# Kernel optimization log

Measured on AMD Instinct MI355X. Metric: run time of the kernel, lower is better.

The kernel has to match this reference:

```python
import jax, jax.numpy as jnp
import numpy as np

T_DIFF = 1000.0
LN_EPS = 1e-5


def _lin(x, w, b):
    return jnp.matmul(x, w.T) + b


def _ln(x, g, b):
    m = jnp.mean(x, axis=-1, keepdims=True)
    v = jnp.mean((x - m) ** 2, axis=-1, keepdims=True)
    return (x - m) / jnp.sqrt(v + LN_EPS) * g + b


def _pos_lin(x, w, b):
    return jnp.matmul(x, jax.nn.softplus(w).T) + b


def _gamma(t, g_l1_w, g_l1_b, g_l2_w, g_l2_b, g_l3_w, g_l3_b, gamma_0, gamma_1):
    def gtilde(u):
        l1 = _pos_lin(u, g_l1_w, g_l1_b)
        return l1 + _pos_lin(jax.nn.sigmoid(_pos_lin(l1, g_l2_w, g_l2_b)), g_l3_w, g_l3_b)
    g0, g1, gt = gtilde(jnp.zeros_like(t)), gtilde(jnp.ones_like(t)), gtilde(t)
    return gamma_0 + (gamma_1 - gamma_0) * (gt - g0) / (g1 - g0)


def _pair_dist(a):
    # safe pairwise euclidean distances, (B,N,N,1)
    diff = a[:, :, None, :] - a[:, None, :, :]
    d2 = jnp.sum(diff * diff, axis=-1, keepdims=True)
    return diff, jnp.sqrt(jnp.maximum(d2, 1e-12)), d2


def _egc_layer(x, h, x0, p):
    _, d0, _ = _pair_dist(x0)                      # original distances
    diff, dist, d2 = _pair_dist(x)                 # current distances (pre-LN x)
    h = _ln(h, p['lnh_g'], p['lnh_b'])
    x = _ln(x, p['lnx_g'], p['lnx_b'])
    B, N, F = h.shape
    h_i = jnp.broadcast_to(h[:, :, None, :], (B, N, N, F))
    h_j = jnp.broadcast_to(h[:, None, :, :], (B, N, N, F))
    einp = jnp.concatenate([h_i, h_j, d2, d0], axis=-1)  # (B,N,N,2F+2)
    m = jax.nn.silu(_lin(einp, p['edg1_w'], p['edg1_b']))
    m = jax.nn.silu(_lin(m, p['edg2_w'], p['edg2_b']))
    e = jax.nn.sigmoid(_lin(m, p['edgi_w'], p['edgi_b']))
    e = e * (1.0 - jnp.eye(N, dtype=e.dtype)[None, :, :, None])
    m_agg = jnp.sum(e * m, axis=2)                 # sum over j -> (B,N,F)
    hn = jax.nn.silu(_lin(jnp.concatenate([h, m_agg], axis=-1), p['node1_w'], p['node1_b']))
    hn = h + _lin(hn, p['node2_w'], p['node2_b'])
    cw = jax.nn.silu(_lin(einp, p['cor1_w'], p['cor1_b']))
    cw = jax.nn.silu(_lin(cw, p['cor2_w'], p['cor2_b']))
    cw = _lin(cw, p['cor3_w'], p['cor3_b'])        # (B,N,N,1)
    x_next = x + jnp.sum(cw * (diff / (dist + 1.0)), axis=2)
    return x_next, hn


def setup_inputs() -> dict:
    key = jax.random.key(0)
    ks = iter(jax.random.split(key, 64))
    B, N, H, L = 8, 192, 32, 4
    d = {}
    d['xyz_atom_species'] = jax.random.normal(next(ks), (B, N, 4), jnp.float32)
    d['pdf'] = jax.random.normal(next(ks), (B, 3000), jnp.float32)
    d['t'] = jax.random.uniform(next(ks), (B,), jnp.float32) * T_DIFF

    def w(k, shape):
        fan_in = shape[-1]
        return jax.random.normal(k, shape, jnp.float32) / np.sqrt(fan_in)

    d['emb_in_w'] = w(next(ks), (H, 12)); d['emb_in_b'] = jnp.zeros((H,), jnp.float32)
    d['emb_out_w'] = w(next(ks), (1, H)); d['emb_out_b'] = jnp.zeros((1,), jnp.float32)
    d['x_out_w'] = w(next(ks), (3, 3)); d['x_out_b'] = jnp.zeros((3,), jnp.float32)
    d['pdf_w'] = w(next(ks), (10, 3000)); d['pdf_b'] = jnp.zeros((10,), jnp.float32)
    d['g_l1_w'] = w(next(ks), (1, 1)); d['g_l1_b'] = jnp.zeros((1,), jnp.float32)
    d['g_l2_w'] = w(next(ks), (1024, 1)); d['g_l2_b'] = jnp.zeros((1024,), jnp.float32)
    d['g_l3_w'] = w(next(ks), (1, 1024)); d['g_l3_b'] = jnp.zeros((1,), jnp.float32)
    d['gamma_0'] = jnp.array([-5.0], jnp.float32)
    d['gamma_1'] = jnp.array([10.0], jnp.float32)
    d['lnh_g'] = jnp.ones((L, H), jnp.float32); d['lnh_b'] = jnp.zeros((L, H), jnp.float32)
    d['lnx_g'] = jnp.ones((L, 3), jnp.float32); d['lnx_b'] = jnp.zeros((L, 3), jnp.float32)
    d['edg1_w'] = w(next(ks), (L, H, 2 * H + 2)); d['edg1_b'] = jnp.zeros((L, H), jnp.float32)
    d['edg2_w'] = w(next(ks), (L, H, H)); d['edg2_b'] = jnp.zeros((L, H), jnp.float32)
    d['edgi_w'] = w(next(ks), (L, 1, H)); d['edgi_b'] = jnp.zeros((L, 1), jnp.float32)
    d['node1_w'] = w(next(ks), (L, H, 2 * H)); d['node1_b'] = jnp.zeros((L, H), jnp.float32)
    d['node2_w'] = w(next(ks), (L, H, H)); d['node2_b'] = jnp.zeros((L, H), jnp.float32)
    d['cor1_w'] = w(next(ks), (L, H, 2 * H + 2)); d['cor1_b'] = jnp.zeros((L, H), jnp.float32)
    d['cor2_w'] = w(next(ks), (L, H, H)); d['cor2_b'] = jnp.zeros((L, H), jnp.float32)
    d['cor3_w'] = w(next(ks), (L, 1, H)); d['cor3_b'] = jnp.zeros((L, 1), jnp.float32)
    return d


def reference(xyz_atom_species, pdf, t, emb_in_w, emb_in_b, emb_out_w, emb_out_b,
              x_out_w, x_out_b, pdf_w, pdf_b, g_l1_w, g_l1_b, g_l2_w, g_l2_b,
              g_l3_w, g_l3_b, gamma_0, gamma_1, lnh_g, lnh_b, lnx_g, lnx_b,
              edg1_w, edg1_b, edg2_w, edg2_b, edgi_w, edgi_b, node1_w, node1_b,
              node2_w, node2_b, cor1_w, cor1_b, cor2_w, cor2_b, cor3_w, cor3_b):
    B, N, _ = xyz_atom_species.shape
    h = xyz_atom_species[:, :, 3:4]                # (B,N,1)
    x = xyz_atom_species[:, :, :3]
    x0 = x
    tn = (t / T_DIFF)[:, None]                     # (B,1)
    t_emb = _gamma(tn, g_l1_w, g_l1_b, g_l2_w, g_l2_b, g_l3_w, g_l3_b, gamma_0, gamma_1)
    pdf_emb = _lin(pdf, pdf_w, pdf_b)              # (B,10)
    h = jnp.concatenate([
        h,
        jnp.broadcast_to(t_emb[:, None, :], (B, N, 1)),
        jnp.broadcast_to(pdf_emb[:, None, :], (B, N, 10)),
    ], axis=-1)
    h = _lin(h, emb_in_w, emb_in_b)                # (B,N,32)
    for l in range(4):
        p = dict(lnh_g=lnh_g[l], lnh_b=lnh_b[l], lnx_g=lnx_g[l], lnx_b=lnx_b[l],
                 edg1_w=edg1_w[l], edg1_b=edg1_b[l], edg2_w=edg2_w[l], edg2_b=edg2_b[l],
                 edgi_w=edgi_w[l], edgi_b=edgi_b[l], node1_w=node1_w[l], node1_b=node1_b[l],
                 node2_w=node2_w[l], node2_b=node2_b[l], cor1_w=cor1_w[l], cor1_b=cor1_b[l],
                 cor2_w=cor2_w[l], cor2_b=cor2_b[l], cor3_w=cor3_w[l], cor3_b=cor3_b[l])
        x, h = _egc_layer(x, h, x0, p)
    h = _lin(h, emb_out_w, emb_out_b)
    x = _lin(x, x_out_w, x_out_b) - x0
    return jnp.concatenate([x, h], axis=-1)        # (B,N,4)
```

## Files before the change

kernel.cpp:

```cpp
#include <hip/hip_runtime.h>
#include <hip/hip_bf16.h>
#include <math.h>

#define BATCH 8
#define NATOMS 192
#define HF 32

using short8 = __attribute__((ext_vector_type(8))) short;
using f32x4  = __attribute__((ext_vector_type(4))) float;

__device__ __forceinline__ float fast_rcp(float x){ return __builtin_amdgcn_rcpf(x); }
__device__ __forceinline__ float sigmoid_f(float x){ return fast_rcp(1.0f+__expf(-x)); }
__device__ __forceinline__ float silu_f(float x){ return x*fast_rcp(1.0f+__expf(-x)); }
__device__ __forceinline__ float softplus_f(float x){ return fmaxf(x,0.0f)+log1pf(expf(-fabsf(x))); }
__device__ __forceinline__ unsigned short f2bf(float x){
  __hip_bfloat16 h = __float2bfloat16(x);
  return __builtin_bit_cast(unsigned short, h);
}

__device__ __forceinline__ float wave_sum(float v){
  v += __shfl_xor(v, 1);
  v += __shfl_xor(v, 2);
  v += __shfl_xor(v, 4);
  v += __shfl_xor(v, 8);
  v += __shfl_xor(v, 16);
  v += __shfl_xor(v, 32);
  return v;
}

__global__ __launch_bounds__(256) void k_prelude(
    const float* __restrict__ pdf, const float* __restrict__ t,
    const float* __restrict__ pdf_w, const float* __restrict__ pdf_b,
    const float* __restrict__ g1w, const float* __restrict__ g1b,
    const float* __restrict__ g2w, const float* __restrict__ g2b,
    const float* __restrict__ g3w, const float* __restrict__ g3b,
    const float* __restrict__ gamma0, const float* __restrict__ gamma1,
    float* __restrict__ temb, float* __restrict__ pdfe)
{
  __shared__ float lds[4];
  const int bx = blockIdx.x, tid = threadIdx.x;
  const int wv = tid >> 6, ln = tid & 63;

  if (bx < 80){
    const int b = bx / 10, o = bx % 10;
    const float* pb = pdf + b*3000;
    const float* wb = pdf_w + o*3000;
    float p = 0.f;
    for (int k = tid; k < 3000; k += 256) p = fmaf(pb[k], wb[k], p);
    p = wave_sum(p);
    if (ln == 0) lds[wv] = p;
    __syncthreads();
    if (tid == 0) pdfe[b*10 + o] = lds[0] + lds[1] + lds[2] + lds[3] + pdf_b[o];
    return;
  }
  const int b = bx - 80;
  const float w1 = softplus_f(g1w[0]);
  const float b1 = g1b[0];
  const float tn = t[b] * (1.0f/1000.0f);
  const float l1_0 = b1;
  const float l1_1 = w1 + b1;
  const float l1_t = fmaf(w1, tn, b1);
  float a0 = 0.f, a1 = 0.f, at = 0.f;
  for (int k = tid; k < 1024; k += 256){
    float w2 = softplus_f(g2w[k]);
    float bb = g2b[k];
    float w3 = softplus_f(g3w[k]);
    a0 += sigmoid_f(fmaf(w2, l1_0, bb)) * w3;
    a1 += sigmoid_f(fmaf(w2, l1_1, bb)) * w3;
    at += sigmoid_f(fmaf(w2, l1_t, bb)) * w3;
  }
  float sums[3]; float vals[3] = {a0, a1, at};
  for (int r = 0; r < 3; ++r){
    float v = wave_sum(vals[r]);
    __syncthreads();
    if (ln == 0) lds[wv] = v;
    __syncthreads();
    sums[r] = lds[0] + lds[1] + lds[2] + lds[3];
  }
  if (tid == 0){
    const float b3 = g3b[0];
    const float g0 = l1_0 + sums[0] + b3;
    const float g1v = l1_1 + sums[1] + b3;
    const float gt = l1_t + sums[2] + b3;
    temb[b] = gamma0[0] + (gamma1[0] - gamma0[0]) * (gt - g0) / (g1v - g0);
  }
}

__global__ __launch_bounds__(256) void k_embed(
    const float* __restrict__ xyz, const float* __restrict__ temb,
    const float* __restrict__ pdfe, const float* __restrict__ wi,
    const float* __restrict__ bi, float* __restrict__ h, float* __restrict__ x)
{
  int g = blockIdx.x * 256 + threadIdx.x;
  if (g >= BATCH*NATOMS*HF) return;
  int f = g & 31;
  int node = g >> 5;
  int b = node / NATOMS;
  float sp = xyz[node*4 + 3];
  const float* w = wi + f*12;
  float a = bi[f];
  a = fmaf(sp, w[0], a);
  a = fmaf(temb[b], w[1], a);
  const float* pe = pdfe + b*10;
#pragma unroll
  for (int p = 0; p < 10; ++p) a = fmaf(pe[p], w[2+p], a);
  h[node*32 + f] = a;
  if (f < 3) x[node*3 + f] = xyz[node*4 + f];
}

__global__ __launch_bounds__(256) void k_wprep(
    const float* __restrict__ e2w, const float* __restrict__ c2w,
    unsigned short* __restrict__ e2wb, unsigned short* __restrict__ c2wb)
{
  int g = blockIdx.x*256 + threadIdx.x;
  if (g < 4096){
    e2wb[g] = f2bf(e2w[g]);
    c2wb[g] = f2bf(c2w[g]);
  }
}

__global__ __launch_bounds__(256) void k_node(
    const float* __restrict__ hraw,
    const float* __restrict__ lnhg, const float* __restrict__ lnhb,
    const float* __restrict__ e1w, const float* __restrict__ e1b,
    const float* __restrict__ c1w, const float* __restrict__ c1b,
    float* __restrict__ hln, float* __restrict__ ue, float* __restrict__ uc,
    float* __restrict__ vep, float* __restrict__ vcp)
{
  int g = blockIdx.x * 256 + threadIdx.x;
  if (g >= BATCH*NATOMS*32) return;
  const int f = g & 31, node = g >> 5;
  const float* row = hraw + node*32;
  float hl[32];
  float m = 0.f;
#pragma unroll
  for (int k = 0; k < 32; ++k){ hl[k] = row[k]; m += hl[k]; }
  m *= (1.0f/32.0f);
  float v = 0.f;
#pragma unroll
  for (int k = 0; k < 32; ++k){ float d = hl[k]-m; v = fmaf(d, d, v); }
  float r = rsqrtf(v*(1.0f/32.0f) + 1e-5f);
#pragma unroll
  for (int k = 0; k < 32; ++k) hl[k] = fmaf((hl[k]-m)*r, lnhg[k], lnhb[k]);
  hln[node*32 + f] = hl[f];

  const float* we = e1w + f*66;
  float sv = e1b[f], su = 0.f;
#pragma unroll
  for (int k = 0; k < 32; ++k){ sv = fmaf(hl[k], we[k], sv); su = fmaf(hl[k], we[32+k], su); }
  vep[node*32 + f] = sv;
  ue [node*32 + f] = su;

  const float* wc = c1w + f*66;
  float cv = c1b[f], cu = 0.f;
#pragma unroll
  for (int k = 0; k < 32; ++k){ cv = fmaf(hl[k], wc[k], cv); cu = fmaf(hl[k], wc[32+k], cu); }
  vcp[node*32 + f] = cv;
  uc [node*32 + f] = cu;
}

__global__ __launch_bounds__(128, 3) void k_pair(
    const float* __restrict__ xin, const float* __restrict__ xyz,
    const float* __restrict__ ue, const float* __restrict__ uc,
    const float* __restrict__ vep, const float* __restrict__ vcp,
    const float* __restrict__ e1w, const float* __restrict__ c1w,
    const unsigned short* __restrict__ e2wb, const unsigned short* __restrict__ c2wb,
    const float* __restrict__ e2b, const float* __restrict__ eiw,
    const float* __restrict__ eib,
    const float* __restrict__ c2b, const float* __restrict__ c3w,
    const float* __restrict__ c3b,
    float* __restrict__ pm, float* __restrict__ pxc)
{
  __shared__ float s_geo[64][6];
  __shared__ unsigned short s_m1[64][40];
  __shared__ unsigned short s_c1[64][40];
  __shared__ unsigned short s_we[32][40];
  __shared__ unsigned short s_wc[32][40];

  const int i = blockIdx.x, b = blockIdx.y, chunk = blockIdx.z;
  const int tid = threadIdx.x;
  const int base = b * NATOMS;

  if (tid < 64){
    const int jj = tid;
    const int j = chunk*64 + jj;
    const float* xi_p = xin + (base + i)*3;
    const float* xj_p = xin + (base + j)*3;
    const float dfx = xi_p[0] - xj_p[0], dfy = xi_p[1] - xj_p[1], dfz = xi_p[2] - xj_p[2];
    const float d2 = dfx*dfx + dfy*dfy + dfz*dfz;
    const float dist = sqrtf(fmaxf(d2, 1e-12f));
    const float* x0i = xyz + (base + i)*4;
    const float* x0j = xyz + (base + j)*4;
    const float q0 = x0i[0]-x0j[0], q1 = x0i[1]-x0j[1], q2 = x0i[2]-x0j[2];
    const float d0 = sqrtf(fmaxf(q0*q0 + q1*q1 + q2*q2, 1e-12f));
    s_geo[jj][0] = dfx; s_geo[jj][1] = dfy; s_geo[jj][2] = dfz;
    s_geo[jj][3] = d2;  s_geo[jj][4] = d0;  s_geo[jj][5] = dist;
  } else {
    const int u = tid - 64;
    const short8* es = (const short8*)e2wb;
    const short8* cs = (const short8*)c2wb;
#pragma unroll
    for (int h = 0; h < 2; ++h){
      const int c = u + h*64;
      const int f = c >> 2, kq = c & 3;
      *(short8*)&s_we[f][kq*8] = es[c];
      *(short8*)&s_wc[f][kq*8] = cs[c];
    }
  }
  __syncthreads();

  {
    const int k = tid & 31, jg = tid >> 5;
    const float vpe = vep[(base + i)*32 + k];
    const float vpc = vcp[(base + i)*32 + k];
    const float we64 = e1w[k*66 + 64], we65 = e1w[k*66 + 65];
    const float wc64 = c1w[k*66 + 64], wc65 = c1w[k*66 + 65];
#pragma unroll
    for (int jj = jg; jj < 64; jj += 4){
      const float d2 = s_geo[jj][3], d0 = s_geo[jj][4];
      const int j = chunk*64 + jj;
      const float uev = ue[(size_t)(base + j)*32 + k];
      const float m1 = silu_f(fmaf(d2, we64, fmaf(d0, we65, vpe + uev)));
      s_m1[jj][k] = f2bf(m1);
      const float ucv = uc[(size_t)(base + j)*32 + k];
      const float c1 = silu_f(fmaf(d2, wc64, fmaf(d0, wc65, vpc + ucv)));
      s_c1[jj][k] = f2bf(c1);
    }
  }
  __syncthreads();

  const int lane = tid & 63;
  const int n = lane & 15, quad = lane >> 4;

  if (tid < 64){
    short8 b0 = *(const short8*)&s_we[n][quad*8];
    short8 b1 = *(const short8*)&s_we[16 + n][quad*8];
    f32x4 acc0[4], acc1[4];
#pragma unroll
    for (int jt = 0; jt < 4; ++jt){
      short8 a = *(const short8*)&s_m1[jt*16 + n][quad*8];
      f32x4 z = {0.f, 0.f, 0.f, 0.f};
      acc0[jt] = __builtin_amdgcn_mfma_f32_16x16x32_bf16(a, b0, z, 0, 0, 0);
      acc1[jt] = __builtin_amdgcn_mfma_f32_16x16x32_bf16(a, b1, z, 0, 0, 0);
    }
    const float eb0 = e2b[n], eb1 = e2b[16 + n];
    const float ew0 = eiw[n], ew1 = eiw[16 + n];
    const float ebias = eib[0];
    float ma0 = 0.f, ma1 = 0.f;
#pragma unroll
    for (int jt = 0; jt < 4; ++jt){
      float m20[4], m21[4], g[4];
#pragma unroll
      for (int r = 0; r < 4; ++r){
        m20[r] = silu_f(acc0[jt][r] + eb0);
        m21[r] = silu_f(acc1[jt][r] + eb1);
        g[r] = m20[r]*ew0 + m21[r]*ew1;
      }
#pragma unroll
      for (int r = 0; r < 4; ++r){
        g[r] += __shfl_xor(g[r], 1);
        g[r] += __shfl_xor(g[r], 2);
        g[r] += __shfl_xor(g[r], 4);
        g[r] += __shfl_xor(g[r], 8);
      }
#pragma unroll
      for (int r = 0; r < 4; ++r){
        const int jglob = chunk*64 + jt*16 + quad*4 + r;
        const float e = (jglob == i) ? 0.0f : sigmoid_f(g[r] + ebias);
        ma0 = fmaf(e, m20[r], ma0);
        ma1 = fmaf(e, m21[r], ma1);
      }
    }
    ma0 += __shfl_xor(ma0, 16); ma0 += __shfl_xor(ma0, 32);
    ma1 += __shfl_xor(ma1, 16); ma1 += __shfl_xor(ma1, 32);
    if (lane < 16){
      float* o = pm + ((size_t)(base + i)*3 + chunk)*32;
      o[lane] = ma0;
      o[16 + lane] = ma1;
    }
  } else {
    short8 b0 = *(const short8*)&s_wc[n][quad*8];
    short8 b1 = *(const short8*)&s_wc[16 + n][quad*8];
    f32x4 acc0[4], acc1[4];
#pragma unroll
    for (int jt = 0; jt < 4; ++jt){
      short8 a = *(const short8*)&s_c1[jt*16 + n][quad*8];
      f32x4 z = {0.f, 0.f, 0.f, 0.f};
      acc0[jt] = __builtin_amdgcn_mfma_f32_16x16x32_bf16(a, b0, z, 0, 0, 0);
      acc1[jt] = __builtin_amdgcn_mfma_f32_16x16x32_bf16(a, b1, z, 0, 0, 0);
    }
    const float cb0 = c2b[n], cb1 = c2b[16 + n];
    const float cw0 = c3w[n], cw1 = c3w[16 + n];
    const float cbias = c3b[0];
    float px = 0.f, py = 0.f, pz = 0.f;
#pragma unroll
    for (int jt = 0; jt < 4; ++jt){
      float g[4];
#pragma unroll
      for (int r = 0; r < 4; ++r){
        g[r] = silu_f(acc0[jt][r] + cb0)*cw0 + silu_f(acc1[jt][r] + cb1)*cw1;
      }
#pragma unroll
      for (int r = 0; r < 4; ++r){
        g[r] += __shfl_xor(g[r], 1);
        g[r] += __shfl_xor(g[r], 2);
        g[r] += __shfl_xor(g[r], 4);
        g[r] += __shfl_xor(g[r], 8);
      }
#pragma unroll
      for (int r = 0; r < 4; ++r){
        const int jj = jt*16 + quad*4 + r;
        const float s = (g[r] + cbias) * fast_rcp(s_geo[jj][5] + 1.0f);
        px = fmaf(s, s_geo[jj][0], px);
        py = fmaf(s, s_geo[jj][1], py);
        pz = fmaf(s, s_geo[jj][2], pz);
      }
    }
    px += __shfl_xor(px, 16); px += __shfl_xor(px, 32);
    py += __shfl_xor(py, 16); py += __shfl_xor(py, 32);
    pz += __shfl_xor(pz, 16); pz += __shfl_xor(pz, 32);
    if (lane == 0){
      float* o = pxc + ((size_t)(base + i)*3 + chunk)*3;
      o[0] = px; o[1] = py; o[2] = pz;
    }
  }
}

__global__ __launch_bounds__(256) void k_post(
    float* hln, const float* __restrict__ xin,
    const float* __restrict__ pm, const float* __restrict__ pxc,
    float* __restrict__ hout, float* __restrict__ xout,
    const float* __restrict__ n1w, const float* __restrict__ n1b,
    const float* __restrict__ n2w, const float* __restrict__ n2b,
    const float* __restrict__ lnxg, const float* __restrict__ lnxb,
    const float* __restrict__ lnhg_n, const float* __restrict__ lnhb_n,
    const float* __restrict__ e1w_n, const float* __restrict__ e1b_n,
    const float* __restrict__ c1w_n, const float* __restrict__ c1b_n,
    float* __restrict__ ue, float* __restrict__ uc,
    float* __restrict__ vep, float* __restrict__ vcp)
{
  __shared__ float s_hl[8][33];
  __shared__ float s_mg[8][33];
  __shared__ float s_n1[8][33];
  __shared__ float s_ho[8][33];

  const int tid = threadIdx.x;
  const int il = tid >> 5, f = tid & 31;
  const int node = blockIdx.x*8 + il;

  const float hlf = hln[node*32 + f];
  s_hl[il][f] = hlf;
  const float* pmn = pm + (size_t)node*96;
  s_mg[il][f] = pmn[f] + pmn[32 + f] + pmn[64 + f];
  __syncthreads();

  float a = n1b[f];
  const float* w1 = n1w + f*64;
#pragma unroll
  for (int k = 0; k < 32; ++k) a = fmaf(s_hl[il][k], w1[k], a);
#pragma unroll
  for (int k = 0; k < 32; ++k) a = fmaf(s_mg[il][k], w1[32+k], a);
  s_n1[il][f] = silu_f(a);

  if (f < 3){
    const float* xr = xin + node*3;
    const float x0 = xr[0], x1 = xr[1], x2 = xr[2];
    const float mx = (x0 + x1 + x2) * (1.0f/3.0f);
    const float v0 = x0-mx, v1 = x1-mx, v2 = x2-mx;
    const float r = rsqrtf((v0*v0 + v1*v1 + v2*v2)*(1.0f/3.0f) + 1e-5f);
    const float xv = (f == 0) ? x0 : ((f == 1) ? x1 : x2);
    const float xl = fmaf((xv - mx)*r, lnxg[f], lnxb[f]);
    const float* pc = pxc + (size_t)node*9;
    xout[node*3 + f] = xl + pc[f] + pc[3 + f] + pc[6 + f];
  }
  __syncthreads();

  float o = n2b[f];
  const float* w2 = n2w + f*32;
#pragma unroll
  for (int k = 0; k < 32; ++k) o = fmaf(s_n1[il][k], w2[k], o);
  const float ho = hlf + o;
  hout[node*32 + f] = ho;
  s_ho[il][f] = ho;
  __syncthreads();

  float m = 0.f;
#pragma unroll
  for (int k = 0; k < 32; ++k) m += s_ho[il][k];
  m *= (1.0f/32.0f);
  float v = 0.f;
#pragma unroll
  for (int k = 0; k < 32; ++k){ float d = s_ho[il][k]-m; v = fmaf(d, d, v); }
  const float r = rsqrtf(v*(1.0f/32.0f) + 1e-5f);
  float hl[32];
#pragma unroll
  for (int k = 0; k < 32; ++k) hl[k] = fmaf((s_ho[il][k]-m)*r, lnhg_n[k], lnhb_n[k]);
  hln[node*32 + f] = hl[f];

  const float* we = e1w_n + f*66;
  float sv = e1b_n[f], su = 0.f;
#pragma unroll
  for (int k = 0; k < 32; ++k){ sv = fmaf(hl[k], we[k], sv); su = fmaf(hl[k], we[32+k], su); }
  vep[node*32 + f] = sv;
  ue [node*32 + f] = su;

  const float* wc = c1w_n + f*66;
  float cv = c1b_n[f], cu = 0.f;
#pragma unroll
  for (int k = 0; k < 32; ++k){ cv = fmaf(hl[k], wc[k], cv); cu = fmaf(hl[k], wc[32+k], cu); }
  vcp[node*32 + f] = cv;
  uc [node*32 + f] = cu;
}

__global__ __launch_bounds__(256) void k_final(
    const float* __restrict__ hin, const float* __restrict__ xin,
    const float* __restrict__ xyz,
    const float* __restrict__ how, const float* __restrict__ hob,
    const float* __restrict__ xow, const float* __restrict__ xob,
    float* __restrict__ out)
{
  int g = blockIdx.x * 256 + threadIdx.x;
  if (g >= BATCH*NATOMS) return;
  const float* h = hin + g*32;
  float a = hob[0];
#pragma unroll
  for (int k = 0; k < 32; ++k) a = fmaf(h[k], how[k], a);
  const float* x = xin + g*3;
#pragma unroll
  for (int c = 0; c < 3; ++c){
    float o = xob[c];
    o = fmaf(x[0], xow[c*3+0], o);
    o = fmaf(x[1], xow[c*3+1], o);
    o = fmaf(x[2], xow[c*3+2], o);
    out[g*4 + c] = o - xyz[g*4 + c];
  }
  out[g*4 + 3] = a;
}

extern "C" void kernel_launch(void* const* d_in, const int* in_sizes, int n_in,
                              void* d_out, int out_size, void* d_ws, size_t ws_size,
                              hipStream_t stream)
{
  const float* xyz      = (const float*)d_in[0];
  const float* pdf      = (const float*)d_in[1];
  const float* t        = (const float*)d_in[2];
  const float* emb_in_w = (const float*)d_in[3];
  const float* emb_in_b = (const float*)d_in[4];
  const float* emb_out_w= (const float*)d_in[5];
  const float* emb_out_b= (const float*)d_in[6];
  const float* x_out_w  = (const float*)d_in[7];
  const float* x_out_b  = (const float*)d_in[8];
  const float* pdf_w    = (const float*)d_in[9];
  const float* pdf_b    = (const float*)d_in[10];
  const float* g1w      = (const float*)d_in[11];
  const float* g1b      = (const float*)d_in[12];
  const float* g2w      = (const float*)d_in[13];
  const float* g2b      = (const float*)d_in[14];
  const float* g3w      = (const float*)d_in[15];
  const float* g3b      = (const float*)d_in[16];
  const float* gamma0   = (const float*)d_in[17];
  const float* gamma1   = (const float*)d_in[18];
  const float* lnhg     = (const float*)d_in[19];
  const float* lnhb     = (const float*)d_in[20];
  const float* lnxg     = (const float*)d_in[21];
  const float* lnxb     = (const float*)d_in[22];
  const float* e1w      = (const float*)d_in[23];
  const float* e1b      = (const float*)d_in[24];
  const float* e2w      = (const float*)d_in[25];
  const float* e2b      = (const float*)d_in[26];
  const float* eiw      = (const float*)d_in[27];
  const float* eib      = (const float*)d_in[28];
  const float* n1w      = (const float*)d_in[29];
  const float* n1b      = (const float*)d_in[30];
  const float* n2w      = (const float*)d_in[31];
  const float* n2b      = (const float*)d_in[32];
  const float* c1w      = (const float*)d_in[33];
  const float* c1b      = (const float*)d_in[34];
  const float* c2w      = (const float*)d_in[35];
  const float* c2b      = (const float*)d_in[36];
  const float* c3w      = (const float*)d_in[37];
  const float* c3b      = (const float*)d_in[38];

  const int NTOT = BATCH*NATOMS;
  float* ws   = (float*)d_ws;
  float* temb = ws;
  float* pdfe = ws + 8;
  unsigned short* e2wb = (unsigned short*)(ws + 96);
  unsigned short* c2wb = e2wb + 4096;
  float* h0   = ws + 96 + 4096;
  float* hout = h0   + NTOT*32;
  float* xb0  = hout + NTOT*32;
  float* xb1  = xb0  + NTOT*3;
  float* hln  = xb1  + NTOT*3;
  float* ue   = hln  + NTOT*32;
  float* uc   = ue   + NTOT*32;
  float* vep  = uc   + NTOT*32;
  float* vcp  = vep  + NTOT*32;
  float* pm   = vcp  + NTOT*32;
  float* pxc  = pm   + NTOT*96;

  k_prelude<<<88, 256, 0, stream>>>(pdf, t, pdf_w, pdf_b,
      g1w, g1b, g2w, g2b, g3w, g3b, gamma0, gamma1, temb, pdfe);
  k_embed<<<(NTOT*HF + 255)/256, 256, 0, stream>>>(
      xyz, temb, pdfe, emb_in_w, emb_in_b, h0, xb0);
  k_wprep<<<16, 256, 0, stream>>>(e2w, c2w, e2wb, c2wb);
  k_node<<<(NTOT*32 + 255)/256, 256, 0, stream>>>(
      h0, lnhg, lnhb, e1w, e1b, c1w, c1b, hln, ue, uc, vep, vcp);

  const float* xcur = xb0; float* xnext = xb1;
  for (int l = 0; l < 4; ++l){
    const int n = (l < 3) ? (l + 1) : 3;
    k_pair<<<dim3(NATOMS, BATCH, 3), 128, 0, stream>>>(
        xcur, xyz, ue, uc, vep, vcp,
        e1w + l*2112, c1w + l*2112,
        e2wb + l*1024, c2wb + l*1024,
        e2b + l*32, eiw + l*32, eib + l,
        c2b + l*32, c3w + l*32, c3b + l,
        pm, pxc);
    k_post<<<NTOT/8, 256, 0, stream>>>(
        hln, xcur, pm, pxc, hout, xnext,
        n1w + l*2048, n1b + l*32, n2w + l*1024, n2b + l*32,
        lnxg + l*3, lnxb + l*3,
        lnhg + n*32, lnhb + n*32, e1w + n*2112, e1b + n*32,
        c1w + n*2112, c1b + n*32,
        ue, uc, vep, vcp);
    const float* tx = xcur; xcur = xnext; xnext = (float*)tx;
  }

  k_final<<<(NTOT + 255)/256, 256, 0, stream>>>(
      hout, xcur, xyz, emb_out_w, emb_out_b, x_out_w, x_out_b, (float*)d_out);
}
```

Before: 274.9 us.

## Fuse node update into pair kernel via last-block atomic counter, merge prelude kernels

After: 926.0 us. 237% more time.

```diff
diff --git a/kernel.cpp b/kernel.cpp
--- a/kernel.cpp
+++ b/kernel.cpp
@@ -35,12 +35,20 @@
     const float* __restrict__ g2w, const float* __restrict__ g2b,
     const float* __restrict__ g3w, const float* __restrict__ g3b,
     const float* __restrict__ gamma0, const float* __restrict__ gamma1,
+    const float* __restrict__ e2w, const float* __restrict__ c2w,
+    unsigned short* __restrict__ e2wb, unsigned short* __restrict__ c2wb,
     float* __restrict__ temb, float* __restrict__ pdfe)
 {
   __shared__ float lds[4];
   const int bx = blockIdx.x, tid = threadIdx.x;
   const int wv = tid >> 6, ln = tid & 63;
 
+  if (bx >= 88){
+    const int g = (bx - 88)*256 + tid;
+    e2wb[g] = f2bf(e2w[g]);
+    c2wb[g] = f2bf(c2w[g]);
+    return;
+  }
   if (bx < 80){
     const int b = bx / 10, o = bx % 10;
     const float* pb = pdf + b*3000;
@@ -86,55 +94,43 @@
   }
 }
 
-__global__ __launch_bounds__(256) void k_embed(
+__global__ __launch_bounds__(256) void k_embed_node(
     const float* __restrict__ xyz, const float* __restrict__ temb,
     const float* __restrict__ pdfe, const float* __restrict__ wi,
-    const float* __restrict__ bi, float* __restrict__ h, float* __restrict__ x)
-{
-  int g = blockIdx.x * 256 + threadIdx.x;
-  if (g >= BATCH*NATOMS*HF) return;
-  int f = g & 31;
-  int node = g >> 5;
-  int b = node / NATOMS;
-  float sp = xyz[node*4 + 3];
-  const float* w = wi + f*12;
-  float a = bi[f];
-  a = fmaf(sp, w[0], a);
-  a = fmaf(temb[b], w[1], a);
-  const float* pe = pdfe + b*10;
-#pragma unroll
-  for (int p = 0; p < 10; ++p) a = fmaf(pe[p], w[2+p], a);
-  h[node*32 + f] = a;
-  if (f < 3) x[node*3 + f] = xyz[node*4 + f];
-}
-
-__global__ __launch_bounds__(256) void k_wprep(
-    const float* __restrict__ e2w, const float* __restrict__ c2w,
-    unsigned short* __restrict__ e2wb, unsigned short* __restrict__ c2wb)
-{
-  int g = blockIdx.x*256 + threadIdx.x;
-  if (g < 4096){
-    e2wb[g] = f2bf(e2w[g]);
-    c2wb[g] = f2bf(c2w[g]);
-  }
-}
-
-__global__ __launch_bounds__(256) void k_node(
-    const float* __restrict__ hraw,
+    const float* __restrict__ bi,
     const float* __restrict__ lnhg, const float* __restrict__ lnhb,
     const float* __restrict__ e1w, const float* __restrict__ e1b,
     const float* __restrict__ c1w, const float* __restrict__ c1b,
-    float* __restrict__ hln, float* __restrict__ ue, float* __restrict__ uc,
-    float* __restrict__ vep, float* __restrict__ vcp)
+    float* __restrict__ x, float* __restrict__ hln,
+    float* __restrict__ ue, float* __restrict__ uc,
+    float* __restrict__ vep, float* __restrict__ vcp,
+    int* __restrict__ cnt)
 {
-  int g = blockIdx.x * 256 + threadIdx.x;
-  if (g >= BATCH*NATOMS*32) return;
-  const int f = g & 31, node = g >> 5;
-  const float* row = hraw + node*32;
+  __shared__ float s_h[8][33];
+  const int tid = threadIdx.x;
+  const int il = tid >> 5, f = tid & 31;
+  const int node = blockIdx.x*8 + il;
+  const int b = node / NATOMS;
+
+  {
+    const float sp = xyz[node*4 + 3];
+    const float* w = wi + f*12;
+    float a = bi[f];
+    a = fmaf(sp, w[0], a);
+    a = fmaf(temb[b], w[1], a);
+    const float* pe = pdfe + b*10;
+#pragma unroll
+    for (int p = 0; p < 10; ++p) a = fmaf(pe[p], w[2+p], a);
+    s_h[il][f] = a;
+  }
+  if (f < 3) x[node*3 + f] = xyz[node*4 + f];
+  if (f == 0) cnt[node] = 0;
+  __syncthreads();
+
   float hl[32];
   float m = 0.f;
 #pragma unroll
-  for (int k = 0; k < 32; ++k){ hl[k] = row[k]; m += hl[k]; }
+  for (int k = 0; k < 32; ++k){ hl[k] = s_h[il][k]; m += hl[k]; }
   m *= (1.0f/32.0f);
   float v = 0.f;
 #pragma unroll
@@ -161,21 +157,35 @@
 
 __global__ __launch_bounds__(128, 3) void k_pair(
     const float* __restrict__ xin, const float* __restrict__ xyz,
-    const float* __restrict__ ue, const float* __restrict__ uc,
-    const float* __restrict__ vep, const float* __restrict__ vcp,
+    const float* __restrict__ hln, const float* __restrict__ ue,
+    const float* __restrict__ uc, const float* __restrict__ vep,
+    const float* __restrict__ vcp,
     const float* __restrict__ e1w, const float* __restrict__ c1w,
     const unsigned short* __restrict__ e2wb, const unsigned short* __restrict__ c2wb,
     const float* __restrict__ e2b, const float* __restrict__ eiw,
     const float* __restrict__ eib,
     const float* __restrict__ c2b, const float* __restrict__ c3w,
     const float* __restrict__ c3b,
-    float* __restrict__ pm, float* __restrict__ pxc)
+    const float* __restrict__ n1w, const float* __restrict__ n1b,
+    const float* __restrict__ n2w, const float* __restrict__ n2b,
+    const float* __restrict__ lnxg, const float* __restrict__ lnxb,
+    const float* __restrict__ lnhg_n, const float* __restrict__ lnhb_n,
+    const float* __restrict__ e1w_n, const float* __restrict__ e1b_n,
+    const float* __restrict__ c1w_n, const float* __restrict__ c1b_n,
+    float* __restrict__ hln_n, float* __restrict__ ue_n,
+    float* __restrict__ uc_n, float* __restrict__ vep_n,
+    float* __restrict__ vcp_n, float* __restrict__ xout,
+    const float* __restrict__ how, const float* __restrict__ hob,
+    const float* __restrict__ xow, const float* __restrict__ xob,
+    float* __restrict__ dout, const int lastl,
+    float* __restrict__ pm, float* __restrict__ pxc, int* __restrict__ cnt)
 {
   __shared__ float s_geo[64][6];
   __shared__ unsigned short s_m1[64][40];
   __shared__ unsigned short s_c1[64][40];
   __shared__ unsigned short s_we[32][40];
   __shared__ unsigned short s_wc[32][40];
+  __shared__ int s_last;
 
   const int i = blockIdx.x, b = blockIdx.y, chunk = blockIdx.z;
   const int tid = threadIdx.x;
@@ -324,117 +334,99 @@
       o[0] = px; o[1] = py; o[2] = pz;
     }
   }
-}
-
-__global__ __launch_bounds__(256) void k_post(
-    float* hln, const float* __restrict__ xin,
-    const float* __restrict__ pm, const float* __restrict__ pxc,
-    float* __restrict__ hout, float* __restrict__ xout,
-    const float* __restrict__ n1w, const float* __restrict__ n1b,
-    const float* __restrict__ n2w, const float* __restrict__ n2b,
-    const float* __restrict__ lnxg, const float* __restrict__ lnxb,
-    const float* __restrict__ lnhg_n, const float* __restrict__ lnhb_n,
-    const float* __restrict__ e1w_n, const float* __restrict__ e1b_n,
-    const float* __restrict__ c1w_n, const float* __restrict__ c1b_n,
-    float* __restrict__ ue, float* __restrict__ uc,
-    float* __restrict__ vep, float* __restrict__ vcp)
-{
-  __shared__ float s_hl[8][33];
-  __shared__ float s_mg[8][33];
-  __shared__ float s_n1[8][33];
-  __shared__ float s_ho[8][33];
-
-  const int tid = threadIdx.x;
-  const int il = tid >> 5, f = tid & 31;
-  const int node = blockIdx.x*8 + il;
-
+
+  __threadfence();
+  if (tid == 0){
+    const int old = atomicAdd(&cnt[base + i], 1);
+    s_last = (old == 2) ? 1 : 0;
+  }
+  __syncthreads();
+  if (!s_last) return;
+  if (tid >= 64) return;
+  __threadfence();
+
+  const int f = tid & 31;
+  const int node = base + i;
+
+  const float* pmn = pm + (size_t)node*96;
+  const float mgf = pmn[f] + pmn[32 + f] + pmn[64 + f];
   const float hlf = hln[node*32 + f];
-  s_hl[il][f] = hlf;
-  const float* pmn = pm + (size_t)node*96;
-  s_mg[il][f] = pmn[f] + pmn[32 + f] + pmn[64 + f];
-  __syncthreads();
 
   float a = n1b[f];
   const float* w1 = n1w + f*64;
 #pragma unroll
-  for (int k = 0; k < 32; ++k) a = fmaf(s_hl[il][k], w1[k], a);
-#pragma unroll
-  for (int k = 0; k < 32; ++k) a = fmaf(s_mg[il][k], w1[32+k], a);
-  s_n1[il][f] = silu_f(a);
-
-  if (f < 3){
+  for (int k = 0; k < 32; ++k) a = fmaf(__shfl(hlf, k, 64), w1[k], a);
+#pragma unroll
+  for (int k = 0; k < 32; ++k) a = fmaf(__shfl(mgf, k, 64), w1[32 + k], a);
+  const float n1v = silu_f(a);
+  float o = n2b[f];
+  const float* w2 = n2w + f*32;
+#pragma unroll
+  for (int k = 0; k < 32; ++k) o = fmaf(__shfl(n1v, k, 64), w2[k], o);
+  const float ho = hlf + o;
+
+  float xn0, xn1, xn2;
+  {
     const float* xr = xin + node*3;
     const float x0 = xr[0], x1 = xr[1], x2 = xr[2];
     const float mx = (x0 + x1 + x2) * (1.0f/3.0f);
     const float v0 = x0-mx, v1 = x1-mx, v2 = x2-mx;
     const float r = rsqrtf((v0*v0 + v1*v1 + v2*v2)*(1.0f/3.0f) + 1e-5f);
-    const float xv = (f == 0) ? x0 : ((f == 1) ? x1 : x2);
-    const float xl = fmaf((xv - mx)*r, lnxg[f], lnxb[f]);
     const float* pc = pxc + (size_t)node*9;
-    xout[node*3 + f] = xl + pc[f] + pc[3 + f] + pc[6 + f];
-  }
-  __syncthreads();
-
-  float o = n2b[f];
-  const float* w2 = n2w + f*32;
-#pragma unroll
-  for (int k = 0; k < 32; ++k) o = fmaf(s_n1[il][k], w2[k], o);
-  const float ho = hlf + o;
-  hout[node*32 + f] = ho;
-  s_ho[il][f] = ho;
-  __syncthreads();
-
-  float m = 0.f;
-#pragma unroll
-  for (int k = 0; k < 32; ++k) m += s_ho[il][k];
-  m *= (1.0f/32.0f);
-  float v = 0.f;
-#pragma unroll
-  for (int k = 0; k < 32; ++k){ float d = s_ho[il][k]-m; v = fmaf(d, d, v); }
-  const float r = rsqrtf(v*(1.0f/32.0f) + 1e-5f);
-  float hl[32];
-#pragma unroll
-  for (int k = 0; k < 32; ++k) hl[k] = fmaf((s_ho[il][k]-m)*r, lnhg_n[k], lnhb_n[k]);
-  hln[node*32 + f] = hl[f];
-
-  const float* we = e1w_n + f*66;
-  float sv = e1b_n[f], su = 0.f;
-#pragma unroll
-  for (int k = 0; k < 32; ++k){ sv = fmaf(hl[k], we[k], sv); su = fmaf(hl[k], we[32+k], su); }
-  vep[node*32 + f] = sv;
-  ue [node*32 + f] = su;
-
-  const float* wc = c1w_n + f*66;
-  float cv = c1b_n[f], cu = 0.f;
-#pragma unroll
-  for (int k = 0; k < 32; ++k){ cv = fmaf(hl[k], wc[k], cv); cu = fmaf(hl[k], wc[32+k], cu); }
-  vcp[node*32 + f] = cv;
-  uc [node*32 + f] = cu;
-}
-
-__global__ __launch_bounds__(256) void k_final(
-    const float* __restrict__ hin, const float* __restrict__ xin,
-    const float* __restrict__ xyz,
-    const float* __restrict__ how, const float* __restrict__ hob,
-    const float* __restrict__ xow, const float* __restrict__ xob,
-    float* __restrict__ out)
-{
-  int g = blockIdx.x * 256 + threadIdx.x;
-  if (g >= BATCH*NATOMS) return;
-  const float* h = hin + g*32;
-  float a = hob[0];
-#pragma unroll
-  for (int k = 0; k < 32; ++k) a = fmaf(h[k], how[k], a);
-  const float* x = xin + g*3;
-#pragma unroll
-  for (int c = 0; c < 3; ++c){
-    float o = xob[c];
-    o = fmaf(x[0], xow[c*3+0], o);
-    o = fmaf(x[1], xow[c*3+1], o);
-    o = fmaf(x[2], xow[c*3+2], o);
-    out[g*4 + c] = o - xyz[g*4 + c];
-  }
-  out[g*4 + 3] = a;
+    xn0 = fmaf(v0*r, lnxg[0], lnxb[0]) + pc[0] + pc[3] + pc[6];
+    xn1 = fmaf(v1*r, lnxg[1], lnxb[1]) + pc[1] + pc[4] + pc[7];
+    xn2 = fmaf(v2*r, lnxg[2], lnxb[2]) + pc[2] + pc[5] + pc[8];
+  }
+
+  if (!lastl){
+    if (tid == 0){
+      float* xo = xout + node*3;
+      xo[0] = xn0; xo[1] = xn1; xo[2] = xn2;
+    }
+    float s = ho;
+    s += __shfl_xor(s, 1); s += __shfl_xor(s, 2); s += __shfl_xor(s, 4);
+    s += __shfl_xor(s, 8); s += __shfl_xor(s, 16);
+    const float m = s * (1.0f/32.0f);
+    const float d = ho - m;
+    float vv = d*d;
+    vv += __shfl_xor(vv, 1); vv += __shfl_xor(vv, 2); vv += __shfl_xor(vv, 4);
+    vv += __shfl_xor(vv, 8); vv += __shfl_xor(vv, 16);
+    const float r = rsqrtf(vv*(1.0f/32.0f) + 1e-5f);
+    const float hl = fmaf(d*r, lnhg_n[f], lnhb_n[f]);
+    if (tid < 32) hln_n[node*32 + f] = hl;
+
+    const float* we = e1w_n + f*66;
+    const float* wc = c1w_n + f*66;
+    float sv = e1b_n[f], su = 0.f, cv = c1b_n[f], cu = 0.f;
+#pragma unroll
+    for (int k = 0; k < 32; ++k){
+      const float tkk = __shfl(hl, k, 64);
+      sv = fmaf(tkk, we[k], sv);
+      su = fmaf(tkk, we[32 + k], su);
+      cv = fmaf(tkk, wc[k], cv);
+      cu = fmaf(tkk, wc[32 + k], cu);
+    }
+    if (tid < 32){
+      vep_n[node*32 + f] = sv;
+      ue_n [node*32 + f] = su;
+      vcp_n[node*32 + f] = cv;
+      uc_n [node*32 + f] = cu;
+    }
+  } else {
+    float hh = how[f] * ho;
+    hh += __shfl_xor(hh, 1); hh += __shfl_xor(hh, 2); hh += __shfl_xor(hh, 4);
+    hh += __shfl_xor(hh, 8); hh += __shfl_xor(hh, 16);
+    if (tid == 0) dout[node*4 + 3] = hh + hob[0];
+    if (tid < 3){
+      const int c = tid;
+      float oo = xob[c];
+      oo = fmaf(xn0, xow[c*3 + 0], oo);
+      oo = fmaf(xn1, xow[c*3 + 1], oo);
+      oo = fmaf(xn2, xow[c*3 + 2], oo);
+      dout[node*4 + c] = oo - xyz[node*4 + c];
+    }
+  }
+  if (tid == 0) cnt[node] = 0;
 }
 
 extern "C" void kernel_launch(void* const* d_in, const int* in_sizes, int n_in,
@@ -487,46 +479,48 @@
   float* pdfe = ws + 8;
   unsigned short* e2wb = (unsigned short*)(ws + 96);
   unsigned short* c2wb = e2wb + 4096;
-  float* h0   = ws + 96 + 4096;
-  float* hout = h0   + NTOT*32;
-  float* xb0  = hout + NTOT*32;
-  float* xb1  = xb0  + NTOT*3;
-  float* hln  = xb1  + NTOT*3;
-  float* ue   = hln  + NTOT*32;
-  float* uc   = ue   + NTOT*32;
-  float* vep  = uc   + NTOT*32;
-  float* vcp  = vep  + NTOT*32;
-  float* pm   = vcp  + NTOT*32;
+  float* p0   = ws + 96 + 4096;
+  float* xbA  = p0;                float* xbB  = xbA + NTOT*3;
+  float* hlnA = xbB  + NTOT*3;     float* hlnB = hlnA + NTOT*32;
+  float* ueA  = hlnB + NTOT*32;    float* ueB  = ueA  + NTOT*32;
+  float* ucA  = ueB  + NTOT*32;    float* ucB  = ucA  + NTOT*32;
+  float* vepA = ucB  + NTOT*32;    float* vepB = vepA + NTOT*32;
+  float* vcpA = vepB + NTOT*32;    float* vcpB = vcpA + NTOT*32;
+  float* pm   = vcpB + NTOT*32;
   float* pxc  = pm   + NTOT*96;
-
-  k_prelude<<<88, 256, 0, stream>>>(pdf, t, pdf_w, pdf_b,
-      g1w, g1b, g2w, g2b, g3w, g3b, gamma0, gamma1, temb, pdfe);
-  k_embed<<<(NTOT*HF + 255)/256, 256, 0, stream>>>(
-      xyz, temb, pdfe, emb_in_w, emb_in_b, h0, xb0);
-  k_wprep<<<16, 256, 0, stream>>>(e2w, c2w, e2wb, c2wb);
-  k_node<<<(NTOT*32 + 255)/256, 256, 0, stream>>>(
-      h0, lnhg, lnhb, e1w, e1b, c1w, c1b, hln, ue, uc, vep, vcp);
-
-  const float* xcur = xb0; float* xnext = xb1;
+  int*   cnt  = (int*)(pxc + NTOT*9);
+
+  float* xb[2]  = {xbA,  xbB};
+  float* hlnP[2]= {hlnA, hlnB};
+  float* ueP[2] = {ueA,  ueB};
+  float* ucP[2] = {ucA,  ucB};
+  float* vepP[2]= {vepA, vepB};
+  float* vcpP[2]= {vcpA, vcpB};
+
+  k_prelude<<<104, 256, 0, stream>>>(pdf, t, pdf_w, pdf_b,
+      g1w, g1b, g2w, g2b, g3w, g3b, gamma0, gamma1,
+      e2w, c2w, e2wb, c2wb, temb, pdfe);
+  k_embed_node<<<NTOT/8, 256, 0, stream>>>(
+      xyz, temb, pdfe, emb_in_w, emb_in_b,
+      lnhg, lnhb, e1w, e1b, c1w, c1b,
+      xbA, hlnA, ueA, ucA, vepA, vcpA, cnt);
+
   for (int l = 0; l < 4; ++l){
-    const int n = (l < 3) ? (l + 1) : 3;
+    const int p = l & 1;
+    const int nl = (l < 3) ? (l + 1) : 3;
     k_pair<<<dim3(NATOMS, BATCH, 3), 128, 0, stream>>>(
-        xcur, xyz, ue, uc, vep, vcp,
+        xb[p], xyz, hlnP[p], ueP[p], ucP[p], vepP[p], vcpP[p],
         e1w + l*2112, c1w + l*2112,
         e2wb + l*1024, c2wb + l*1024,
         e2b + l*32, eiw + l*32, eib + l,
         c2b + l*32, c3w + l*32, c3b + l,
-        pm, pxc);
-    k_post<<<NTOT/8, 256, 0, stream>>>(
-        hln, xcur, pm, pxc, hout, xnext,
         n1w + l*2048, n1b + l*32, n2w + l*1024, n2b + l*32,
         lnxg + l*3, lnxb + l*3,
-        lnhg + n*32, lnhb + n*32, e1w + n*2112, e1b + n*32,
-        c1w + n*2112, c1b + n*32,
-        ue, uc, vep, vcp);
-    const float* tx = xcur; xcur = xnext; xnext = (float*)tx;
-  }
-
-  k_final<<<(NTOT + 255)/256, 256, 0, stream>>>(
-      hout, xcur, xyz, emb_out_w, emb_out_b, x_out_w, x_out_b, (float*)d_out);
+        lnhg + nl*32, lnhb + nl*32,
+        e1w + nl*2112, e1b + nl*32, c1w + nl*2112, c1b + nl*32,
+        hlnP[1-p], ueP[1-p], ucP[1-p], vepP[1-p], vcpP[1-p], xb[1-p],
+        emb_out_w, emb_out_b, x_out_w, x_out_b,
+        (float*)d_out, (l == 3) ? 1 : 0,
+        pm, pxc, cnt);
+  }
 }
```
